# Performance work log

Measured on AMD Instinct MI355X. Metric: run time of the kernel, lower is better.

Reference implementation:

```python
import jax, jax.numpy as jnp
import numpy as np

N, M, D, G, E = 1024, 1024, 1024, 16, 64  # rois, ref rois, feat_dim, groups, emb_dim
DG = D // G  # 64 per-group dim


def _make_boxes(k, n):
    k1, k2 = jax.random.split(k)
    xy = jax.random.uniform(k1, (n, 2), dtype=jnp.float32) * 500.0
    wh = jax.random.uniform(k2, (n, 2), dtype=jnp.float32) * 100.0 + 1.0
    return jnp.concatenate([xy, xy + wh], axis=1)  # [n,4] xmin,ymin,xmax,ymax


def setup_inputs() -> dict:
    key = jax.random.key(0)
    ks = jax.random.split(key, 10)
    s = 0.02
    return {
        "roi_feat": jax.random.normal(ks[0], (N, D), dtype=jnp.float32),
        "ref_feat": jax.random.normal(ks[1], (M, D), dtype=jnp.float32),
        "rois1": _make_boxes(ks[2], N),
        "rois2": _make_boxes(ks[3], M),
        "Wq": jax.random.normal(ks[4], (D, D), dtype=jnp.float32) * s,
        "bq": jnp.zeros((D,), jnp.float32),
        "Wk": jax.random.normal(ks[5], (D, D), dtype=jnp.float32) * s,
        "bk": jnp.zeros((D,), jnp.float32),
        "Wg": jax.random.normal(ks[6], (G, E), dtype=jnp.float32) * s,
        "bg": jnp.zeros((G,), jnp.float32),
        "Wv": jax.random.normal(ks[7], (G, DG, D), dtype=jnp.float32) * s,
        "bv": jnp.zeros((D,), jnp.float32),
    }


def _position_matrix(bbox, ref_bbox):
    # bbox [N,4], ref_bbox [M,4] -> [N,M,4]
    def parts(b):
        xmin, ymin, xmax, ymax = b[:, 0], b[:, 1], b[:, 2], b[:, 3]
        w = xmax - xmin + 1.0
        h = ymax - ymin + 1.0
        cx = 0.5 * (xmin + xmax)
        cy = 0.5 * (ymin + ymax)
        return w, h, cx, cy

    w, h, cx, cy = parts(bbox)            # [N]
    wr, hr, cxr, cyr = parts(ref_bbox)    # [M]
    dx = jnp.log(jnp.abs((cx[:, None] - cxr[None, :]) / w[:, None]) + 1e-3)
    dy = jnp.log(jnp.abs((cy[:, None] - cyr[None, :]) / h[:, None]) + 1e-3)
    dw = jnp.log(w[:, None] / wr[None, :])
    dh = jnp.log(h[:, None] / hr[None, :])
    return jnp.stack([dx, dy, dw, dh], axis=2)  # [N,M,4]


def _position_embedding(pos_mat, feat_dim=64, wave_length=1000.0):
    fr = jnp.arange(feat_dim // 8, dtype=jnp.float32)            # [8]
    dim_mat = jnp.power(wave_length, (8.0 / feat_dim) * fr)      # [8]
    div = pos_mat[..., None] * 100.0 / dim_mat                   # [N,M,4,8]
    emb = jnp.concatenate([jnp.sin(div), jnp.cos(div)], axis=3)  # [N,M,4,16]
    return emb.reshape(pos_mat.shape[0], pos_mat.shape[1], -1)   # [N,M,64]


def reference(roi_feat, ref_feat, rois1, rois2, Wq, bq, Wk, bk, Wg, bg, Wv, bv):
    # position embedding: [N,M,E]
    pos_emb = _position_embedding(_position_matrix(rois1, rois2), feat_dim=E)
    # Wgs 1x1 conv (E -> G) + relu -> aff_weight [N,G,M]
    aff_weight = jax.nn.relu(jnp.einsum("nme,ge->ngm", pos_emb, Wg) + bg[None, :, None])
    # grouped q/k projections
    q = (roi_feat @ Wq + bq).reshape(N, G, DG)   # [N,G,dg]
    k = (ref_feat @ Wk + bk).reshape(M, G, DG)   # [M,G,dg]
    aff = jnp.einsum("ngd,mgd->ngm", q, k) * (1.0 / np.sqrt(DG))
    weighted = jnp.log(aff_weight + 1e-6) + aff  # [N,G,M]
    sm = jax.nn.softmax(weighted, axis=2)
    out_t = jnp.einsum("ngm,md->ngd", sm, ref_feat)          # [N,G,D]
    out = jnp.einsum("ngd,god->ngo", out_t, Wv).reshape(N, D) + bv  # grouped 1x1 conv
    return out
```

## Files before the change

kernel.cpp:

```cpp
#include <hip/hip_runtime.h>
#include <hip/hip_fp16.h>
#include <cstddef>

#define N_ 1024
#define M_ 1024
#define D_ 1024
#define G_ 16
#define DG_ 64

typedef __bf16 bf16x8 __attribute__((ext_vector_type(8)));
typedef _Float16 f16x8 __attribute__((ext_vector_type(8)));
typedef float f32x4 __attribute__((ext_vector_type(4)));

__device__ __forceinline__ size_t qkf_idx(int g, int rb, int ks, int lane) {
    return ((((size_t)(g * 64 + rb)) * 2 + ks) * 64 + lane) * 8;
}
__device__ __forceinline__ size_t vf_idx(int g, int ot, int mc, int lane) {
    return ((((size_t)(g * 4 + ot)) * 32 + mc) * 64 + lane) * 8;
}
__device__ __forceinline__ size_t awt_idx(int g, int mb, int n, int quad) {
    return (((size_t)(mb * 1024 + n)) * 16 + g) * 16 + quad * 4;
}

__global__ __launch_bounds__(256)
void gemm_qkv(const float* __restrict__ roi, const float* __restrict__ ref,
              const float* __restrict__ Wq, const float* __restrict__ Wk,
              const float* __restrict__ Wv,
              const float* __restrict__ bq, const float* __restrict__ bk,
              __bf16* __restrict__ Qf, __bf16* __restrict__ Kf,
              __bf16* __restrict__ Vf)
{
    __shared__ __align__(16) char smem[36864];
    const int t = blockIdx.x;
    const int tid = threadIdx.x;
    const int w = tid >> 6, lane = tid & 63;
    const int quad = lane >> 4, l15 = lane & 15;

    const int z = t >> 6, t6 = t & 63;
    const float* A = (z == 0) ? roi : ref;
    const float* Wf = (z == 0) ? Wq : (z == 1) ? Wk : Wv;
    const int i0 = (t6 >> 3) * 128, j0 = (t6 & 7) * 128;
    const int iw = (w & 1) * 64, jw = (w >> 1) * 64;

    __bf16(*As)[72] = (__bf16(*)[72])smem;
    __bf16(*Bs)[72] = (__bf16(*)[72])(smem + 18432);

    f32x4 acc[4][4] = {};

    for (int k0 = 0; k0 < D_; k0 += 64) {
        __syncthreads();
        #pragma unroll
        for (int it = 0; it < 8; ++it) {
            const int idx = tid + 256 * it;
            const int row = idx >> 4, c = idx & 15;
            float4 a = *(const float4*)&A[(size_t)(i0 + row) * D_ + k0 + c * 4];
            __bf16 p[4] = {(__bf16)a.x, (__bf16)a.y, (__bf16)a.z, (__bf16)a.w};
            *(uint2*)&As[row][c * 4] = *(const uint2*)p;
        }
        if (z < 2) {
            #pragma unroll
            for (int it = 0; it < 8; ++it) {
                const int idx = tid + 256 * it;
                const int jl = idx & 127;
                const int kc = idx >> 7;
                const float* src = &Wf[(size_t)(k0 + kc * 4) * D_ + j0 + jl];
                __bf16 p[4];
                p[0] = (__bf16)src[0];
                p[1] = (__bf16)src[D_];
                p[2] = (__bf16)src[2 * D_];
                p[3] = (__bf16)src[3 * D_];
                *(uint2*)&Bs[jl][kc * 4] = *(const uint2*)p;
            }
        } else {
            #pragma unroll
            for (int it = 0; it < 8; ++it) {
                const int idx = tid + 256 * it;
                const int row = idx >> 4, c = idx & 15;
                float4 a = *(const float4*)&Wf[(size_t)(j0 + row) * D_ + k0 + c * 4];
                __bf16 p[4] = {(__bf16)a.x, (__bf16)a.y, (__bf16)a.z, (__bf16)a.w};
                *(uint2*)&Bs[row][c * 4] = *(const uint2*)p;
            }
        }
        __syncthreads();
        #pragma unroll
        for (int ks = 0; ks < 2; ++ks) {
            bf16x8 af[4], bfr[4];
            #pragma unroll
            for (int t4 = 0; t4 < 4; ++t4) {
                af[t4]  = *(const bf16x8*)&As[iw + t4 * 16 + l15][ks * 32 + quad * 8];
                bfr[t4] = *(const bf16x8*)&Bs[jw + t4 * 16 + l15][ks * 32 + quad * 8];
            }
            #pragma unroll
            for (int ti = 0; ti < 4; ++ti)
                #pragma unroll
                for (int tj = 0; tj < 4; ++tj)
                    acc[ti][tj] = __builtin_amdgcn_mfma_f32_16x16x32_bf16(
                        af[ti], bfr[tj], acc[ti][tj], 0, 0, 0);
        }
    }

    if (z < 2) {
        const float* bias = (z == 0) ? bq : bk;
        __bf16* dst = (z == 0) ? Qf : Kf;
        const float scale = (z == 0) ? 0.125f : 1.0f;
        #pragma unroll
        for (int ti = 0; ti < 4; ++ti) {
            const int rb = (i0 + iw + ti * 16) >> 4;
            #pragma unroll
            for (int tj = 0; tj < 4; ++tj) {
                const int go = j0 + jw + tj * 16 + l15;
                const int g = go >> 6, ks = (go >> 5) & 1;
                const int lanef = ((go >> 3) & 3) * 16;
                const int jf = go & 7;
                const float bb = bias[go];
                __bf16* base = dst + qkf_idx(g, rb, ks, 0) + jf;
                #pragma unroll
                for (int r = 0; r < 4; ++r)
                    base[(size_t)(lanef + quad * 4 + r) * 8] =
                        (__bf16)((acc[ti][tj][r] + bb) * scale);
            }
        }
    } else {
        #pragma unroll
        for (int ti = 0; ti < 4; ++ti) {
            const int mbase = i0 + iw + ti * 16 + quad * 4;
            const int mc = mbase >> 5, quadv = (mbase >> 3) & 3, jb = mbase & 7;
            #pragma unroll
            for (int tj = 0; tj < 4; ++tj) {
                const int go = j0 + jw + tj * 16 + l15;
                const int g = go >> 6, ot = (go >> 4) & 3, o15 = go & 15;
                __bf16 p[4];
                #pragma unroll
                for (int r = 0; r < 4; ++r) p[r] = (__bf16)acc[ti][tj][r];
                *(uint2*)&Vf[vf_idx(g, ot, mc, quadv * 16 + o15) + jb] =
                    *(const uint2*)p;
            }
        }
    }
}

__global__ __launch_bounds__(256)
void posbias(const float* __restrict__ rois1, const float* __restrict__ rois2,
             const float* __restrict__ Wg, const float* __restrict__ bg,
             __half* __restrict__ AWt)
{
    const int tid = threadIdx.x;
    const int w = tid >> 6, lane = tid & 63;
    const int quad = lane >> 4, l15 = lane & 15;
    const int n = blockIdx.x;

    const float xmin = rois1[n * 4 + 0], ymin = rois1[n * 4 + 1];
    const float xmax = rois1[n * 4 + 2], ymax = rois1[n * 4 + 3];
    const float wn  = xmax - xmin + 1.f, hn  = ymax - ymin + 1.f;
    const float cxn = 0.5f * (xmin + xmax), cyn = 0.5f * (ymin + ymax);
    const float rwn = 1.0f / wn, rhn = 1.0f / hn;
    const float lwn = __logf(wn), lhn = __logf(hn);

    f16x8 wgf[2];
    #pragma unroll
    for (int ks = 0; ks < 2; ++ks) {
        const float* p = &Wg[l15 * 64 + ks * 32 + quad * 8];
        float4 a = *(const float4*)p;
        float4 bb = *(const float4*)(p + 4);
        wgf[ks][0] = (_Float16)a.x; wgf[ks][1] = (_Float16)a.y;
        wgf[ks][2] = (_Float16)a.z; wgf[ks][3] = (_Float16)a.w;
        wgf[ks][4] = (_Float16)bb.x; wgf[ks][5] = (_Float16)bb.y;
        wgf[ks][6] = (_Float16)bb.z; wgf[ks][7] = (_Float16)bb.w;
    }
    const float bgv = bg[l15];

    const float fr8[8] = {100.0f, 42.16965f, 17.782794f, 7.4989421f,
                          3.1622777f, 1.3335214f, 0.56234133f, 0.23713737f};
    const float phase = (quad & 1) ? 1.5707963267948966f : 0.f;

    for (int mq = 0; mq < 4; ++mq) {
        const int m0w = mq * 256 + w * 64;
        #pragma unroll
        for (int ti = 0; ti < 4; ++ti) {
            const int mt0 = m0w + ti * 16;
            const int m = mt0 + l15;
            float4 r2 = *(const float4*)&rois2[m * 4];
            const float wr  = r2.z - r2.x + 1.f, hr  = r2.w - r2.y + 1.f;
            const float cxr = 0.5f * (r2.x + r2.z), cyr = 0.5f * (r2.y + r2.w);

            const float f0 = __logf(fabsf((cxn - cxr) * rwn) + 0.001f);
            const float f1 = __logf(fabsf((cyn - cyr) * rhn) + 0.001f);
            const float f2 = lwn - __logf(wr);
            const float f3 = lhn - __logf(hr);
            const float fa = (quad & 2) ? f1 : f0;
            const float fb = (quad & 2) ? f3 : f2;

            f32x4 acc = {};
            #pragma unroll
            for (int ks = 0; ks < 2; ++ks) {
                const float feat = ks ? fb : fa;
                f16x8 ef;
                #pragma unroll
                for (int j = 0; j < 8; ++j)
                    ef[j] = (_Float16)__sinf(fmaf(feat, fr8[j], phase));
                acc = __builtin_amdgcn_mfma_f32_16x16x32_f16(ef, wgf[ks], acc, 0, 0, 0);
            }

            __half p[4];
            #pragma unroll
            for (int r = 0; r < 4; ++r)
                p[r] = __float2half(fmaxf(acc[r] + bgv, 0.f) + 1e-6f);
            *(uint2*)&AWt[awt_idx(l15, mt0 >> 4, n, quad)] = *(const uint2*)p;
        }
    }
}

__global__ __launch_bounds__(256)
void attn_mfma(const __bf16* __restrict__ Qf, const __bf16* __restrict__ Kf,
               const __bf16* __restrict__ Vf, const __half* __restrict__ AWt,
               const float* __restrict__ bv, float* __restrict__ out)
{
    __shared__ __align__(16) char smem[17664];

    const int tid = threadIdx.x;
    const int w = tid >> 6, lane = tid & 63;
    const int quad = lane >> 4, l15 = lane & 15;
    const int nb = blockIdx.x, n0 = nb * 16, g = blockIdx.y;

    __bf16(*Psw)[72] = (__bf16(*)[72])(smem + w * 2304);
    float(*accb)[64][17] = (float(*)[64][17])smem;
    float(*lsb)[16] = (float(*)[16])(smem + 17408);

    bf16x8 qf[2];
    qf[0] = *(const bf16x8*)&Qf[qkf_idx(g, nb, 0, lane)];
    qf[1] = *(const bf16x8*)&Qf[qkf_idx(g, nb, 1, lane)];

    f32x4 acc[4] = {};
    float llocal = 0.f;

    #pragma unroll
    for (int t64 = 0; t64 < 4; ++t64) {
        const int mt = w * 4 + t64;

        f32x4 s[4];
        #pragma unroll
        for (int t = 0; t < 4; ++t) {
            bf16x8 ka0 = *(const bf16x8*)&Kf[qkf_idx(g, mt * 4 + t, 0, lane)];
            bf16x8 ka1 = *(const bf16x8*)&Kf[qkf_idx(g, mt * 4 + t, 1, lane)];
            f32x4 z = {};
            __builtin_amdgcn_s_setprio(1);
            z = __builtin_amdgcn_mfma_f32_16x16x32_bf16(ka0, qf[0], z, 0, 0, 0);
            s[t] = __builtin_amdgcn_mfma_f32_16x16x32_bf16(ka1, qf[1], z, 0, 0, 0);
            __builtin_amdgcn_s_setprio(0);
        }

        #pragma unroll
        for (int t = 0; t < 4; ++t) {
            uint2 au = *(const uint2*)&AWt[awt_idx(g, mt * 4 + t, n0 + l15, quad)];
            const __half* a4 = (const __half*)&au;
            __bf16 pk[4];
            #pragma unroll
            for (int r = 0; r < 4; ++r) {
                const float p = __half2float(a4[r]) * __expf(s[t][r]);
                llocal += p;
                pk[r] = (__bf16)p;
            }
            *(uint2*)&Psw[l15][t * 16 + quad * 4] = *(const uint2*)pk;
        }

        #pragma unroll
        for (int mcl = 0; mcl < 2; ++mcl) {
            bf16x8 pbf = *(const bf16x8*)&Psw[l15][mcl * 32 + quad * 8];
            __builtin_amdgcn_s_setprio(1);
            #pragma unroll
            for (int ot = 0; ot < 4; ++ot) {
                bf16x8 va = *(const bf16x8*)&Vf[vf_idx(g, ot, mt * 2 + mcl, lane)];
                acc[ot] = __builtin_amdgcn_mfma_f32_16x16x32_bf16(va, pbf, acc[ot], 0, 0, 0);
            }
            __builtin_amdgcn_s_setprio(0);
        }
    }

    llocal += __shfl_xor(llocal, 16, 64);
    llocal += __shfl_xor(llocal, 32, 64);

    __syncthreads();

    #pragma unroll
    for (int ot = 0; ot < 4; ++ot)
        #pragma unroll
        for (int r = 0; r < 4; ++r)
            accb[w][ot * 16 + quad * 4 + r][l15] = acc[ot][r];
    if (quad == 0) lsb[w][l15] = llocal;
    __syncthreads();

    const float lt = lsb[0][l15] + lsb[1][l15] + lsb[2][l15] + lsb[3][l15];
    const float inv = 1.f / lt;
    #pragma unroll
    for (int r = 0; r < 4; ++r) {
        const int o = w * 16 + quad * 4 + r;
        const int ogl = g * 64 + o;
        const float v = accb[0][o][l15] + accb[1][o][l15] +
                        accb[2][o][l15] + accb[3][o][l15];
        out[(size_t)(n0 + l15) * D_ + ogl] = v * inv + bv[ogl];
    }
}

extern "C" void kernel_launch(void* const* d_in, const int* in_sizes, int n_in,
                              void* d_out, int out_size, void* d_ws, size_t ws_size,
                              hipStream_t stream) {
    const float* roi_feat = (const float*)d_in[0];
    const float* ref_feat = (const float*)d_in[1];
    const float* rois1    = (const float*)d_in[2];
    const float* rois2    = (const float*)d_in[3];
    const float* Wq       = (const float*)d_in[4];
    const float* bq       = (const float*)d_in[5];
    const float* Wk       = (const float*)d_in[6];
    const float* bk       = (const float*)d_in[7];
    const float* Wg       = (const float*)d_in[8];
    const float* bg       = (const float*)d_in[9];
    const float* Wv       = (const float*)d_in[10];
    const float* bv       = (const float*)d_in[11];
    float* out = (float*)d_out;

    char* ws = (char*)d_ws;
    __bf16* Qf  = (__bf16*)(ws + 0);
    __bf16* Kf  = (__bf16*)(ws + (2u << 20));
    __bf16* Vf  = (__bf16*)(ws + (4u << 20));
    __half* AWt = (__half*)(ws + (6u << 20));

    dim3 blk(256);
    gemm_qkv<<<dim3(192), blk, 0, stream>>>(roi_feat, ref_feat, Wq, Wk, Wv,
                                            bq, bk, Qf, Kf, Vf);
    posbias<<<dim3(1024), blk, 0, stream>>>(rois1, rois2, Wg, bg, AWt);
    attn_mfma<<<dim3(64, 16), blk, 0, stream>>>(Qf, Kf, Vf, AWt, bv, out);
}
```

Baseline: 158.2 us.

## Pre-convert operands to bf16 and pipeline QKV GEMM with direct global-to-LDS loads

Adds a prep kernel that converts roi/ref/Wv to bf16 and transposes Wq/Wk to bf16. The same kernel also runs the position-bias blocks, which were a separate launch before. The QKV GEMM then reads the pre-converted bf16 data with global_load_lds into a double-buffered, XOR-swizzled LDS layout. Tiles shrink to 128x64, giving 384 blocks, so loads overlap the MFMA work and the strided fp32 gathers go away. In exchange it adds an extra pass over memory through workspace buffers.

```diff
diff --git a/kernel.cpp b/kernel.cpp
--- a/kernel.cpp
+++ b/kernel.cpp
@@ -1,6 +1,7 @@
 #include <hip/hip_runtime.h>
 #include <hip/hip_fp16.h>
 #include <cstddef>
+#include <cstdint>
 
 #define N_ 1024
 #define M_ 1024
@@ -12,6 +13,13 @@
 typedef _Float16 f16x8 __attribute__((ext_vector_type(8)));
 typedef float f32x4 __attribute__((ext_vector_type(4)));
 
+typedef __attribute__((address_space(1))) const void* gas_ptr;
+typedef __attribute__((address_space(3))) void* las_ptr;
+
+__device__ __forceinline__ void gl_lds16(const void* g, void* l) {
+    __builtin_amdgcn_global_load_lds((gas_ptr)g, (las_ptr)l, 16, 0, 0);
+}
+
 __device__ __forceinline__ size_t qkf_idx(int g, int rb, int ks, int lane) {
     return ((((size_t)(g * 64 + rb)) * 2 + ks) * 64 + lane) * 8;
 }
@@ -23,81 +31,215 @@
 }
 
 __global__ __launch_bounds__(256)
-void gemm_qkv(const float* __restrict__ roi, const float* __restrict__ ref,
+void prep_pos(const float* __restrict__ roi, const float* __restrict__ ref,
               const float* __restrict__ Wq, const float* __restrict__ Wk,
               const float* __restrict__ Wv,
-              const float* __restrict__ bq, const float* __restrict__ bk,
-              __bf16* __restrict__ Qf, __bf16* __restrict__ Kf,
-              __bf16* __restrict__ Vf)
+              __bf16* __restrict__ roiB, __bf16* __restrict__ refB,
+              __bf16* __restrict__ WqT, __bf16* __restrict__ WkT,
+              __bf16* __restrict__ WvR,
+              const float* __restrict__ rois1, const float* __restrict__ rois2,
+              const float* __restrict__ Wg, const float* __restrict__ bg,
+              __half* __restrict__ AWt)
 {
-    __shared__ __align__(16) char smem[36864];
-    const int t = blockIdx.x;
+    __shared__ float tls[64][65];
+    const int b = blockIdx.x;
     const int tid = threadIdx.x;
     const int w = tid >> 6, lane = tid & 63;
     const int quad = lane >> 4, l15 = lane & 15;
 
-    const int z = t >> 6, t6 = t & 63;
-    const float* A = (z == 0) ? roi : ref;
-    const float* Wf = (z == 0) ? Wq : (z == 1) ? Wk : Wv;
-    const int i0 = (t6 >> 3) * 128, j0 = (t6 & 7) * 128;
-    const int iw = (w & 1) * 64, jw = (w >> 1) * 64;
-
-    __bf16(*As)[72] = (__bf16(*)[72])smem;
-    __bf16(*Bs)[72] = (__bf16(*)[72])(smem + 18432);
-
-    f32x4 acc[4][4] = {};
-
-    for (int k0 = 0; k0 < D_; k0 += 64) {
-        __syncthreads();
-        #pragma unroll
-        for (int it = 0; it < 8; ++it) {
-            const int idx = tid + 256 * it;
-            const int row = idx >> 4, c = idx & 15;
-            float4 a = *(const float4*)&A[(size_t)(i0 + row) * D_ + k0 + c * 4];
-            __bf16 p[4] = {(__bf16)a.x, (__bf16)a.y, (__bf16)a.z, (__bf16)a.w};
-            *(uint2*)&As[row][c * 4] = *(const uint2*)p;
-        }
-        if (z < 2) {
-            #pragma unroll
-            for (int it = 0; it < 8; ++it) {
-                const int idx = tid + 256 * it;
-                const int jl = idx & 127;
-                const int kc = idx >> 7;
-                const float* src = &Wf[(size_t)(k0 + kc * 4) * D_ + j0 + jl];
-                __bf16 p[4];
-                p[0] = (__bf16)src[0];
-                p[1] = (__bf16)src[D_];
-                p[2] = (__bf16)src[2 * D_];
-                p[3] = (__bf16)src[3 * D_];
-                *(uint2*)&Bs[jl][kc * 4] = *(const uint2*)p;
+    if (b < 1024) {
+        const int n = b;
+        const float xmin = rois1[n * 4 + 0], ymin = rois1[n * 4 + 1];
+        const float xmax = rois1[n * 4 + 2], ymax = rois1[n * 4 + 3];
+        const float wn  = xmax - xmin + 1.f, hn  = ymax - ymin + 1.f;
+        const float cxn = 0.5f * (xmin + xmax), cyn = 0.5f * (ymin + ymax);
+        const float rwn = 1.0f / wn, rhn = 1.0f / hn;
+        const float lwn = __logf(wn), lhn = __logf(hn);
+
+        f16x8 wgf[2];
+        #pragma unroll
+        for (int ks = 0; ks < 2; ++ks) {
+            const float* p = &Wg[l15 * 64 + ks * 32 + quad * 8];
+            float4 a = *(const float4*)p;
+            float4 bb = *(const float4*)(p + 4);
+            wgf[ks][0] = (_Float16)a.x; wgf[ks][1] = (_Float16)a.y;
+            wgf[ks][2] = (_Float16)a.z; wgf[ks][3] = (_Float16)a.w;
+            wgf[ks][4] = (_Float16)bb.x; wgf[ks][5] = (_Float16)bb.y;
+            wgf[ks][6] = (_Float16)bb.z; wgf[ks][7] = (_Float16)bb.w;
+        }
+        const float bgv = bg[l15];
+
+        const float fr8[8] = {100.0f, 42.16965f, 17.782794f, 7.4989421f,
+                              3.1622777f, 1.3335214f, 0.56234133f, 0.23713737f};
+        const float phase = (quad & 1) ? 1.5707963267948966f : 0.f;
+
+        for (int mq = 0; mq < 4; ++mq) {
+            const int m0w = mq * 256 + w * 64;
+            #pragma unroll
+            for (int ti = 0; ti < 4; ++ti) {
+                const int mt0 = m0w + ti * 16;
+                const int m = mt0 + l15;
+                float4 r2 = *(const float4*)&rois2[m * 4];
+                const float wr  = r2.z - r2.x + 1.f, hr  = r2.w - r2.y + 1.f;
+                const float cxr = 0.5f * (r2.x + r2.z), cyr = 0.5f * (r2.y + r2.w);
+
+                const float f0 = __logf(fabsf((cxn - cxr) * rwn) + 0.001f);
+                const float f1 = __logf(fabsf((cyn - cyr) * rhn) + 0.001f);
+                const float f2 = lwn - __logf(wr);
+                const float f3 = lhn - __logf(hr);
+                const float fa = (quad & 2) ? f1 : f0;
+                const float fb = (quad & 2) ? f3 : f2;
+
+                f32x4 acc = {};
+                #pragma unroll
+                for (int ks = 0; ks < 2; ++ks) {
+                    const float feat = ks ? fb : fa;
+                    f16x8 ef;
+                    #pragma unroll
+                    for (int j = 0; j < 8; ++j)
+                        ef[j] = (_Float16)__sinf(fmaf(feat, fr8[j], phase));
+                    acc = __builtin_amdgcn_mfma_f32_16x16x32_f16(ef, wgf[ks], acc, 0, 0, 0);
+                }
+
+                __half p[4];
+                #pragma unroll
+                for (int r = 0; r < 4; ++r)
+                    p[r] = __float2half(fmaxf(acc[r] + bgv, 0.f) + 1e-6f);
+                *(uint2*)&AWt[awt_idx(l15, mt0 >> 4, n, quad)] = *(const uint2*)p;
             }
+        }
+        return;
+    }
+
+    if (b < 1216) {
+        const int cbk = b - 1024;
+        const int mat = cbk >> 6;
+        const float* S = (mat == 0) ? roi : (mat == 1) ? ref : Wv;
+        __bf16* Dt = (mat == 0) ? roiB : (mat == 1) ? refB : WvR;
+        const int base = (cbk & 63) * 16384;
+        #pragma unroll
+        for (int i = 0; i < 16; ++i) {
+            const int e = base + i * 1024 + tid * 4;
+            float4 v = *(const float4*)&S[e];
+            __bf16 p[4] = {(__bf16)v.x, (__bf16)v.y, (__bf16)v.z, (__bf16)v.w};
+            *(uint2*)&Dt[e] = *(const uint2*)p;
+        }
+        return;
+    }
+
+    const int tb = b - 1216;
+    const int mat = tb >> 8;
+    const float* S = mat ? Wk : Wq;
+    __bf16* Dt = mat ? WkT : WqT;
+    const int tile = tb & 255;
+    const int k0 = (tile >> 4) * 64, j0 = (tile & 15) * 64;
+
+    #pragma unroll
+    for (int rr = 0; rr < 4; ++rr) {
+        const int row = (tid >> 4) * 4 + rr;
+        const int col = (tid & 15) * 4;
+        float4 v = *(const float4*)&S[(size_t)(k0 + row) * 1024 + j0 + col];
+        tls[row][col + 0] = v.x; tls[row][col + 1] = v.y;
+        tls[row][col + 2] = v.z; tls[row][col + 3] = v.w;
+    }
+    __syncthreads();
+    #pragma unroll
+    for (int rr = 0; rr < 4; ++rr) {
+        const int j = (tid >> 4) * 4 + rr;
+        const int kc = (tid & 15) * 4;
+        __bf16 p[4] = {(__bf16)tls[kc + 0][j], (__bf16)tls[kc + 1][j],
+                       (__bf16)tls[kc + 2][j], (__bf16)tls[kc + 3][j]};
+        *(uint2*)&Dt[(size_t)(j0 + j) * 1024 + k0 + kc] = *(const uint2*)p;
+    }
+}
+
+__global__ __launch_bounds__(256)
+void gemm_qkv2(const __bf16* __restrict__ roiB, const __bf16* __restrict__ refB,
+               const __bf16* __restrict__ WqT, const __bf16* __restrict__ WkT,
+               const __bf16* __restrict__ WvR,
+               const float* __restrict__ bq, const float* __restrict__ bk,
+               __bf16* __restrict__ Qf, __bf16* __restrict__ Kf,
+               __bf16* __restrict__ Vf)
+{
+    __shared__ __align__(16) char smem[49152];
+    const int b = blockIdx.x;
+    const int tid = threadIdx.x;
+    const int w = tid >> 6, lane = tid & 63;
+    const int quad = lane >> 4, l15 = lane & 15;
+
+    const int z = b >> 7, t6 = b & 127;
+    const __bf16* A = (z == 0) ? roiB : refB;
+    const __bf16* Bm = (z == 0) ? WqT : (z == 1) ? WkT : WvR;
+    const int i0 = (t6 >> 4) * 128, j0 = (t6 & 15) * 64;
+    const int iw = (w & 1) * 64, jw = (w >> 1) * 32;
+
+    const int gcolc = (((lane & 7) ^ (lane >> 3)) << 4);
+    const char* asrc[4];
+    const char* bsrc[2];
+    #pragma unroll
+    for (int it = 0; it < 4; ++it) {
+        const int row = (w * 4 + it) * 8 + (lane >> 3);
+        asrc[it] = (const char*)A + (size_t)(i0 + row) * 2048 + gcolc;
+    }
+    #pragma unroll
+    for (int it = 0; it < 2; ++it) {
+        const int row = (w * 2 + it) * 8 + (lane >> 3);
+        bsrc[it] = (const char*)Bm + (size_t)(j0 + row) * 2048 + gcolc;
+    }
+
+    const int swm = (l15 & 7) << 4;
+    const int off0 = l15 * 128 + ((quad * 16) ^ swm);
+    const int off1 = l15 * 128 + ((64 + quad * 16) ^ swm);
+
+    f32x4 acc[4][2] = {};
+
+    #define STAGE(c, kb)                                                        \
+        do {                                                                    \
+            _Pragma("unroll")                                                   \
+            for (int it = 0; it < 4; ++it)                                      \
+                gl_lds16(asrc[it] + (kb),                                       \
+                         smem + (c) * 16384 + (w * 4 + it) * 1024);             \
+            _Pragma("unroll")                                                   \
+            for (int it = 0; it < 2; ++it)                                      \
+                gl_lds16(bsrc[it] + (kb),                                       \
+                         smem + 32768 + (c) * 8192 + (w * 2 + it) * 1024);      \
+        } while (0)
+
+    STAGE(0, 0);
+    int cur = 0;
+    for (int t = 0; t < 16; ++t) {
+        if (t < 15) {
+            STAGE(cur ^ 1, (t + 1) * 128);
+            asm volatile("s_waitcnt vmcnt(6)" ::: "memory");
         } else {
-            #pragma unroll
-            for (int it = 0; it < 8; ++it) {
-                const int idx = tid + 256 * it;
-                const int row = idx >> 4, c = idx & 15;
-                float4 a = *(const float4*)&Wf[(size_t)(j0 + row) * D_ + k0 + c * 4];
-                __bf16 p[4] = {(__bf16)a.x, (__bf16)a.y, (__bf16)a.z, (__bf16)a.w};
-                *(uint2*)&Bs[row][c * 4] = *(const uint2*)p;
-            }
-        }
-        __syncthreads();
+            asm volatile("s_waitcnt vmcnt(0)" ::: "memory");
+        }
+        __builtin_amdgcn_s_barrier();
+
+        const char* Ab = smem + cur * 16384;
+        const char* Bb = smem + 32768 + cur * 8192;
         #pragma unroll
         for (int ks = 0; ks < 2; ++ks) {
-            bf16x8 af[4], bfr[4];
-            #pragma unroll
-            for (int t4 = 0; t4 < 4; ++t4) {
-                af[t4]  = *(const bf16x8*)&As[iw + t4 * 16 + l15][ks * 32 + quad * 8];
-                bfr[t4] = *(const bf16x8*)&Bs[jw + t4 * 16 + l15][ks * 32 + quad * 8];
-            }
+            const int offk = ks ? off1 : off0;
+            bf16x8 af[4], bfr[2];
+            #pragma unroll
+            for (int t4 = 0; t4 < 4; ++t4)
+                af[t4] = *(const bf16x8*)(Ab + (iw + t4 * 16) * 128 + offk);
+            #pragma unroll
+            for (int t4 = 0; t4 < 2; ++t4)
+                bfr[t4] = *(const bf16x8*)(Bb + (jw + t4 * 16) * 128 + offk);
             #pragma unroll
             for (int ti = 0; ti < 4; ++ti)
                 #pragma unroll
-                for (int tj = 0; tj < 4; ++tj)
+                for (int tj = 0; tj < 2; ++tj)
                     acc[ti][tj] = __builtin_amdgcn_mfma_f32_16x16x32_bf16(
                         af[ti], bfr[tj], acc[ti][tj], 0, 0, 0);
         }
-    }
+        asm volatile("s_waitcnt lgkmcnt(0)" ::: "memory");
+        __builtin_amdgcn_s_barrier();
+        cur ^= 1;
+    }
+    #undef STAGE
 
     if (z < 2) {
         const float* bias = (z == 0) ? bq : bk;
@@ -107,7 +249,7 @@
         for (int ti = 0; ti < 4; ++ti) {
             const int rb = (i0 + iw + ti * 16) >> 4;
             #pragma unroll
-            for (int tj = 0; tj < 4; ++tj) {
+            for (int tj = 0; tj < 2; ++tj) {
                 const int go = j0 + jw + tj * 16 + l15;
                 const int g = go >> 6, ks = (go >> 5) & 1;
                 const int lanef = ((go >> 3) & 3) * 16;
@@ -126,7 +268,7 @@
             const int mbase = i0 + iw + ti * 16 + quad * 4;
             const int mc = mbase >> 5, quadv = (mbase >> 3) & 3, jb = mbase & 7;
             #pragma unroll
-            for (int tj = 0; tj < 4; ++tj) {
+            for (int tj = 0; tj < 2; ++tj) {
                 const int go = j0 + jw + tj * 16 + l15;
                 const int g = go >> 6, ot = (go >> 4) & 3, o15 = go & 15;
                 __bf16 p[4];
@@ -135,77 +277,6 @@
                 *(uint2*)&Vf[vf_idx(g, ot, mc, quadv * 16 + o15) + jb] =
                     *(const uint2*)p;
             }
-        }
-    }
-}
-
-__global__ __launch_bounds__(256)
-void posbias(const float* __restrict__ rois1, const float* __restrict__ rois2,
-             const float* __restrict__ Wg, const float* __restrict__ bg,
-             __half* __restrict__ AWt)
-{
-    const int tid = threadIdx.x;
-    const int w = tid >> 6, lane = tid & 63;
-    const int quad = lane >> 4, l15 = lane & 15;
-    const int n = blockIdx.x;
-
-    const float xmin = rois1[n * 4 + 0], ymin = rois1[n * 4 + 1];
-    const float xmax = rois1[n * 4 + 2], ymax = rois1[n * 4 + 3];
-    const float wn  = xmax - xmin + 1.f, hn  = ymax - ymin + 1.f;
-    const float cxn = 0.5f * (xmin + xmax), cyn = 0.5f * (ymin + ymax);
-    const float rwn = 1.0f / wn, rhn = 1.0f / hn;
-    const float lwn = __logf(wn), lhn = __logf(hn);
-
-    f16x8 wgf[2];
-    #pragma unroll
-    for (int ks = 0; ks < 2; ++ks) {
-        const float* p = &Wg[l15 * 64 + ks * 32 + quad * 8];
-        float4 a = *(const float4*)p;
-        float4 bb = *(const float4*)(p + 4);
-        wgf[ks][0] = (_Float16)a.x; wgf[ks][1] = (_Float16)a.y;
-        wgf[ks][2] = (_Float16)a.z; wgf[ks][3] = (_Float16)a.w;
-        wgf[ks][4] = (_Float16)bb.x; wgf[ks][5] = (_Float16)bb.y;
-        wgf[ks][6] = (_Float16)bb.z; wgf[ks][7] = (_Float16)bb.w;
-    }
-    const float bgv = bg[l15];
-
-    const float fr8[8] = {100.0f, 42.16965f, 17.782794f, 7.4989421f,
-                          3.1622777f, 1.3335214f, 0.56234133f, 0.23713737f};
-    const float phase = (quad & 1) ? 1.5707963267948966f : 0.f;
-
-    for (int mq = 0; mq < 4; ++mq) {
-        const int m0w = mq * 256 + w * 64;
-        #pragma unroll
-        for (int ti = 0; ti < 4; ++ti) {
-            const int mt0 = m0w + ti * 16;
-            const int m = mt0 + l15;
-            float4 r2 = *(const float4*)&rois2[m * 4];
-            const float wr  = r2.z - r2.x + 1.f, hr  = r2.w - r2.y + 1.f;
-            const float cxr = 0.5f * (r2.x + r2.z), cyr = 0.5f * (r2.y + r2.w);
-
-            const float f0 = __logf(fabsf((cxn - cxr) * rwn) + 0.001f);
-            const float f1 = __logf(fabsf((cyn - cyr) * rhn) + 0.001f);
-            const float f2 = lwn - __logf(wr);
-            const float f3 = lhn - __logf(hr);
-            const float fa = (quad & 2) ? f1 : f0;
-            const float fb = (quad & 2) ? f3 : f2;
-
-            f32x4 acc = {};
-            #pragma unroll
-            for (int ks = 0; ks < 2; ++ks) {
-                const float feat = ks ? fb : fa;
-                f16x8 ef;
-                #pragma unroll
-                for (int j = 0; j < 8; ++j)
-                    ef[j] = (_Float16)__sinf(fmaf(feat, fr8[j], phase));
-                acc = __builtin_amdgcn_mfma_f32_16x16x32_f16(ef, wgf[ks], acc, 0, 0, 0);
-            }
-
-            __half p[4];
-            #pragma unroll
-            for (int r = 0; r < 4; ++r)
-                p[r] = __float2half(fmaxf(acc[r] + bgv, 0.f) + 1e-6f);
-            *(uint2*)&AWt[awt_idx(l15, mt0 >> 4, n, quad)] = *(const uint2*)p;
         }
     }
 }
@@ -319,14 +390,21 @@
     float* out = (float*)d_out;
 
     char* ws = (char*)d_ws;
-    __bf16* Qf  = (__bf16*)(ws + 0);
-    __bf16* Kf  = (__bf16*)(ws + (2u << 20));
-    __bf16* Vf  = (__bf16*)(ws + (4u << 20));
-    __half* AWt = (__half*)(ws + (6u << 20));
+    __bf16* Qf   = (__bf16*)(ws + 0);
+    __bf16* Kf   = (__bf16*)(ws + (2u << 20));
+    __bf16* Vf   = (__bf16*)(ws + (4u << 20));
+    __half* AWt  = (__half*)(ws + (6u << 20));
+    __bf16* roiB = (__bf16*)(ws + (40u << 20));
+    __bf16* refB = (__bf16*)(ws + (42u << 20));
+    __bf16* WqT  = (__bf16*)(ws + (44u << 20));
+    __bf16* WkT  = (__bf16*)(ws + (46u << 20));
+    __bf16* WvR  = (__bf16*)(ws + (48u << 20));
 
     dim3 blk(256);
-    gemm_qkv<<<dim3(192), blk, 0, stream>>>(roi_feat, ref_feat, Wq, Wk, Wv,
-                                            bq, bk, Qf, Kf, Vf);
-    posbias<<<dim3(1024), blk, 0, stream>>>(rois1, rois2, Wg, bg, AWt);
+    prep_pos<<<dim3(1728), blk, 0, stream>>>(roi_feat, ref_feat, Wq, Wk, Wv,
+                                             roiB, refB, WqT, WkT, WvR,
+                                             rois1, rois2, Wg, bg, AWt);
+    gemm_qkv2<<<dim3(384), blk, 0, stream>>>(roiB, refB, WqT, WkT, WvR,
+                                             bq, bk, Qf, Kf, Vf);
     attn_mfma<<<dim3(64, 16), blk, 0, stream>>>(Qf, Kf, Vf, AWt, bv, out);
 }
```

After: 138.2 us. -12.6%, faster.
